# Kernel optimization log

Hardware: AMD Instinct MI355X
Metric: run time of the kernel (lower is better)

The kernel has to match this reference:

```python
import jax, jax.numpy as jnp
import numpy as np

INPUT, HIDDEN = 8, 16

def setup_inputs() -> dict:
    key = jax.random.key(0)
    ks = jax.random.split(key, 7)
    s_ih = 1.0 / np.sqrt(HIDDEN)
    x = jax.random.normal(ks[0], (8192, 512, INPUT), dtype=jnp.float32)
    W_ih = jax.random.uniform(ks[1], (HIDDEN, INPUT), jnp.float32, -s_ih, s_ih)
    W_hh = jax.random.uniform(ks[2], (HIDDEN, HIDDEN), jnp.float32, -s_ih, s_ih)
    b_ih = jax.random.uniform(ks[3], (HIDDEN,), jnp.float32, -s_ih, s_ih)
    b_hh = jax.random.uniform(ks[4], (HIDDEN,), jnp.float32, -s_ih, s_ih)
    s_fc = 1.0 / np.sqrt(HIDDEN)
    fc_w = jax.random.uniform(ks[5], (1, HIDDEN), jnp.float32, -s_fc, s_fc)
    fc_b = jax.random.uniform(ks[6], (1,), jnp.float32, -s_fc, s_fc)
    return {"x": x, "W_ih": W_ih, "W_hh": W_hh, "b_ih": b_ih, "b_hh": b_hh, "fc_w": fc_w, "fc_b": fc_b}

def reference(x, W_ih, W_hh, b_ih, b_hh, fc_w, fc_b):
    B, T, _ = x.shape
    # Precompute input projection for all timesteps: [B, T, H]
    xp = jnp.einsum('bti,hi->bth', x, W_ih) + b_ih + b_hh
    h0 = jnp.zeros((B, HIDDEN), dtype=x.dtype)

    def step(h, xt):
        h_new = jnp.tanh(xt + h @ W_hh.T)
        return h_new, None

    h_last, _ = jax.lax.scan(step, h0, jnp.swapaxes(xp, 0, 1))
    return h_last @ fc_w.T + fc_b  # [B, 1]
```

## Files before the change

### kernel.cpp

```cpp
#include <hip/hip_runtime.h>


#define RNN_B   8192
#define RNN_T   512
#define RNN_IN  8
#define RNN_H   16
#define TC      32
#define NB      16
#define XSTRIDE 264
#define HP      20

__global__ __launch_bounds__(256, 2) void rnn_fused_kernel(
    const float* __restrict__ x,
    const float* __restrict__ W_ih,
    const float* __restrict__ W_hh,
    const float* __restrict__ b_ih,
    const float* __restrict__ b_hh,
    const float* __restrict__ fc_w,
    const float* __restrict__ fc_b,
    float* __restrict__ out)
{
    __shared__ float xs[NB * XSTRIDE];
    __shared__ float hbuf[NB * HP];

    const int tid = (int)threadIdx.x;
    const int j   = tid & 15;
    const int g   = tid >> 4;
    const int b0  = (int)blockIdx.x * NB;
    const int b   = b0 + g;

    float whh[RNN_H];
#pragma unroll
    for (int k = 0; k < RNN_H; k += 4) {
        float4 w = *(const float4*)(W_hh + j * RNN_H + k);
        whh[k] = w.x; whh[k+1] = w.y; whh[k+2] = w.z; whh[k+3] = w.w;
    }
    float wih[RNN_IN];
#pragma unroll
    for (int i = 0; i < RNN_IN; i += 4) {
        float4 w = *(const float4*)(W_ih + j * RNN_IN + i);
        wih[i] = w.x; wih[i+1] = w.y; wih[i+2] = w.z; wih[i+3] = w.w;
    }
    const float bias = b_ih[j] + b_hh[j];

    hbuf[g * HP + j] = 0.0f;

    float hlast = 0.0f;

    for (int t0 = 0; t0 < RNN_T; t0 += TC) {
        __syncthreads();
#pragma unroll
        for (int p = 0; p < 4; ++p) {
            int idx = tid + p * 256;
            int row = idx >> 6;
            int off = idx & 63;
            float4 v = *(const float4*)(x + ((size_t)(b0 + row) * RNN_T + t0) * RNN_IN + off * 4);
            *(float4*)(xs + row * XSTRIDE + off * 4) = v;
        }
        __syncthreads();

#pragma unroll 4
        for (int tt = 0; tt < TC; ++tt) {
            const float* xp = xs + g * XSTRIDE + tt * RNN_IN;
            const float4 xa = *(const float4*)(xp);
            const float4 xb = *(const float4*)(xp + 4);
            const float4 h0 = *(const float4*)(hbuf + g * HP + 0);
            const float4 h1 = *(const float4*)(hbuf + g * HP + 4);
            const float4 h2 = *(const float4*)(hbuf + g * HP + 8);
            const float4 h3 = *(const float4*)(hbuf + g * HP + 12);

            float a0 = fmaf(wih[0], xa.x, bias);
            a0 = fmaf(wih[1], xa.y, a0);
            a0 = fmaf(wih[2], xa.z, a0);
            a0 = fmaf(wih[3], xa.w, a0);
            a0 = fmaf(whh[0], h0.x, a0);
            a0 = fmaf(whh[1], h0.y, a0);

            float a1 = wih[4] * xb.x;
            a1 = fmaf(wih[5], xb.y, a1);
            a1 = fmaf(wih[6], xb.z, a1);
            a1 = fmaf(wih[7], xb.w, a1);
            a1 = fmaf(whh[2], h0.z, a1);
            a1 = fmaf(whh[3], h0.w, a1);

            float a2 = whh[4] * h1.x;
            a2 = fmaf(whh[5],  h1.y, a2);
            a2 = fmaf(whh[6],  h1.z, a2);
            a2 = fmaf(whh[7],  h1.w, a2);
            a2 = fmaf(whh[8],  h2.x, a2);
            a2 = fmaf(whh[9],  h2.y, a2);

            float a3 = whh[10] * h2.z;
            a3 = fmaf(whh[11], h2.w, a3);
            a3 = fmaf(whh[12], h3.x, a3);
            a3 = fmaf(whh[13], h3.y, a3);
            a3 = fmaf(whh[14], h3.z, a3);
            a3 = fmaf(whh[15], h3.w, a3);

            const float s = (a0 + a1) + (a2 + a3);

            const float e  = __expf(s + s);
            const float r  = __builtin_amdgcn_rcpf(e + 1.0f);
            const float hn = fmaf(-2.0f, r, 1.0f);

            hbuf[g * HP + j] = hn;
            hlast = hn;
        }
    }

    float v = hlast * fc_w[j];
    v += __shfl_xor(v, 1);
    v += __shfl_xor(v, 2);
    v += __shfl_xor(v, 4);
    v += __shfl_xor(v, 8);
    if (j == 0) out[b] = v + fc_b[0];
}

extern "C" void kernel_launch(void* const* d_in, const int* in_sizes, int n_in,
                              void* d_out, int out_size, void* d_ws, size_t ws_size,
                              hipStream_t stream)
{
    const float* x    = (const float*)d_in[0];
    const float* W_ih = (const float*)d_in[1];
    const float* W_hh = (const float*)d_in[2];
    const float* b_ih = (const float*)d_in[3];
    const float* b_hh = (const float*)d_in[4];
    const float* fc_w = (const float*)d_in[5];
    const float* fc_b = (const float*)d_in[6];
    float* out = (float*)d_out;

    dim3 grid(RNN_B / NB);
    dim3 block(256);
    rnn_fused_kernel<<<grid, block, 0, stream>>>(x, W_ih, W_hh, b_ih, b_hh, fc_w, fc_b, out);
}
```

Before: 239.2 us.

## Rewrite RNN recurrence as per-wave fp16 MFMA with split-precision and async staging

Replaces the scalar FMA recurrence (one thread per hidden unit, shared-memory hidden state) with a single-wavefront-per-block kernel that computes each timestep as two 16x16x32 fp16 MFMAs. Hidden state and weights use hi/lo fp16 splitting to keep accuracy, and tanh is re-expressed as a sigmoid-style exp2/rcp form with its constants folded into the weights and bias. Input tiles are double-buffered through global_load_lds so loading overlaps compute, and the hidden state is exchanged with ds_bpermute instead of LDS stores. The cost is fp16 rounding error through 512 recurrent steps and much smaller blocks, which lowers per-block parallelism.

Result: slower. 266.6 us (+11.4%).

```diff
diff --git a/kernel.cpp b/kernel.cpp
--- a/kernel.cpp
+++ b/kernel.cpp
@@ -1,4 +1,5 @@
 #include <hip/hip_runtime.h>
+#include <stdint.h>
 
 
 #define RNN_B   8192
@@ -6,11 +7,41 @@
 #define RNN_IN  8
 #define RNN_H   16
 #define TC      32
-#define NB      16
-#define XSTRIDE 264
-#define HP      20
+#define NE      16
+#define XROW    260
+#define NTILE   (RNN_T / TC)
+#define BUFSZ   (NE * XROW)
 
-__global__ __launch_bounds__(256, 2) void rnn_fused_kernel(
+typedef __fp16 half8  __attribute__((ext_vector_type(8)));
+typedef __fp16 half2v __attribute__((ext_vector_type(2)));
+typedef float  f32x4  __attribute__((ext_vector_type(4)));
+
+union H8U { half8 v; __fp16 e[8]; uint32_t u[4]; };
+union H2U { half2v h; uint32_t u; };
+
+static __device__ __forceinline__ uint32_t pkh(float a, float b) {
+    H2U t; t.h = __builtin_amdgcn_cvt_pkrtz(a, b); return t.u;
+}
+static __device__ __forceinline__ uint32_t bp32(int addr, uint32_t v) {
+    return (uint32_t)__builtin_amdgcn_ds_bpermute(addr, (int)v);
+}
+
+static __device__ __forceinline__ void stage(const float* __restrict__ x,
+                                             float* lds_base, int b0, int t0,
+                                             int lane)
+{
+#pragma unroll
+    for (int e = 0; e < NE; ++e) {
+        const float* gp = x + ((size_t)(b0 + e) * RNN_T + t0) * RNN_IN + lane * 4;
+        float* lp = lds_base + e * XROW;
+        __builtin_amdgcn_global_load_lds(
+            (const __attribute__((address_space(1))) uint32_t*)gp,
+            (__attribute__((address_space(3))) uint32_t*)lp,
+            16, 0, 0);
+    }
+}
+
+__global__ __launch_bounds__(64) void rnn_mfma_kernel(
     const float* __restrict__ x,
     const float* __restrict__ W_ih,
     const float* __restrict__ W_hh,
@@ -20,100 +51,105 @@
     const float* __restrict__ fc_b,
     float* __restrict__ out)
 {
-    __shared__ float xs[NB * XSTRIDE];
-    __shared__ float hbuf[NB * HP];
+    __shared__ __align__(16) float xs[2 * BUFSZ];
 
-    const int tid = (int)threadIdx.x;
-    const int j   = tid & 15;
-    const int g   = tid >> 4;
-    const int b0  = (int)blockIdx.x * NB;
-    const int b   = b0 + g;
+    const int lane = (int)threadIdx.x;
+    const int col  = lane & 15;
+    const int q    = lane >> 4;
+    const int b0   = (int)blockIdx.x * NE;
+    const bool hi32  = (lane & 32) != 0;
+    const int addr32 = (lane ^ 32) << 2;
+    const float C2 = 2.8853900817779268f;
 
-    float whh[RNN_H];
+    H8U A1, A2;
 #pragma unroll
-    for (int k = 0; k < RNN_H; k += 4) {
-        float4 w = *(const float4*)(W_hh + j * RNN_H + k);
-        whh[k] = w.x; whh[k+1] = w.y; whh[k+2] = w.z; whh[k+3] = w.w;
+    for (int j = 0; j < 8; ++j) {
+        const int i = j >> 1, hb = j & 1;
+        const int u = 4 * ((i < 2) ? q : (q ^ 2)) + 2 * (i & 1) + hb;
+        const float v = -2.0f * C2 * W_hh[col * RNN_H + u];
+        const __fp16 vh = (__fp16)v;
+        A1.e[j] = vh;
+        if (q < 2) A2.e[j] = (__fp16)(v - (float)vh);
     }
-    float wih[RNN_IN];
+    if (q >= 2) {
 #pragma unroll
-    for (int i = 0; i < RNN_IN; i += 4) {
-        float4 w = *(const float4*)(W_ih + j * RNN_IN + i);
-        wih[i] = w.x; wih[i+1] = w.y; wih[i+2] = w.z; wih[i+3] = w.w;
+        for (int j = 0; j < 8; ++j) {
+            const float uu = C2 * W_ih[col * RNN_IN + j];
+            const __fp16 uh = (__fp16)uu;
+            A2.e[j] = (q == 2) ? uh : (__fp16)(uu - (float)uh);
+        }
     }
-    const float bias = b_ih[j] + b_hh[j];
 
-    hbuf[g * HP + j] = 0.0f;
+    f32x4 cb;
+#pragma unroll
+    for (int rr = 0; rr < 4; ++rr) {
+        const int u = 4 * q + rr;
+        float s = 0.0f;
+        for (int k = 0; k < RNN_H; ++k) {
+            const float v = -2.0f * C2 * W_hh[u * RNN_H + k];
+            const __fp16 vh = (__fp16)v;
+            const __fp16 vl = (__fp16)(v - (float)vh);
+            s += (float)vh + (float)vl;
+        }
+        cb[rr] = C2 * (b_ih[u] + b_hh[u]) - 0.5f * s;
+    }
 
-    float hlast = 0.0f;
+    stage(x, xs, b0, 0, lane);
+    __syncthreads();
 
-    for (int t0 = 0; t0 < RNN_T; t0 += TC) {
-        __syncthreads();
-#pragma unroll
-        for (int p = 0; p < 4; ++p) {
-            int idx = tid + p * 256;
-            int row = idx >> 6;
-            int off = idx & 63;
-            float4 v = *(const float4*)(x + ((size_t)(b0 + row) * RNN_T + t0) * RNN_IN + off * 4);
-            *(float4*)(xs + row * XSTRIDE + off * 4) = v;
-        }
-        __syncthreads();
+    uint32_t rh0 = pkh(0.5f, 0.5f), rh1 = pkh(0.5f, 0.5f);
+    uint32_t rl0 = 0u, rl1 = 0u;
+
+    for (int tile = 0; tile < NTILE; ++tile) {
+        const int cur = tile & 1;
+        if (tile + 1 < NTILE)
+            stage(x, xs + (cur ^ 1) * BUFSZ, b0, (tile + 1) * TC, lane);
+
+        const float* xg = xs + cur * BUFSZ + col * XROW;
 
 #pragma unroll 4
         for (int tt = 0; tt < TC; ++tt) {
-            const float* xp = xs + g * XSTRIDE + tt * RNN_IN;
-            const float4 xa = *(const float4*)(xp);
-            const float4 xb = *(const float4*)(xp + 4);
-            const float4 h0 = *(const float4*)(hbuf + g * HP + 0);
-            const float4 h1 = *(const float4*)(hbuf + g * HP + 4);
-            const float4 h2 = *(const float4*)(hbuf + g * HP + 8);
-            const float4 h3 = *(const float4*)(hbuf + g * HP + 12);
+            const float4 xa = *(const float4*)(xg + tt * 8);
+            const float4 xb = *(const float4*)(xg + tt * 8 + 4);
+            const uint32_t xh0 = pkh(xa.x, xa.y), xh1 = pkh(xa.z, xa.w);
+            const uint32_t xh2 = pkh(xb.x, xb.y), xh3 = pkh(xb.z, xb.w);
 
-            float a0 = fmaf(wih[0], xa.x, bias);
-            a0 = fmaf(wih[1], xa.y, a0);
-            a0 = fmaf(wih[2], xa.z, a0);
-            a0 = fmaf(wih[3], xa.w, a0);
-            a0 = fmaf(whh[0], h0.x, a0);
-            a0 = fmaf(whh[1], h0.y, a0);
+            const uint32_t G0h = bp32(addr32, rh0), G1h = bp32(addr32, rh1);
+            const uint32_t G0l = bp32(addr32, rl0), G1l = bp32(addr32, rl1);
 
-            float a1 = wih[4] * xb.x;
-            a1 = fmaf(wih[5], xb.y, a1);
-            a1 = fmaf(wih[6], xb.z, a1);
-            a1 = fmaf(wih[7], xb.w, a1);
-            a1 = fmaf(whh[2], h0.z, a1);
-            a1 = fmaf(whh[3], h0.w, a1);
+            H8U B1, B2;
+            B1.u[0] = hi32 ? rl0 : rh0;  B1.u[1] = hi32 ? rl1 : rh1;
+            B1.u[2] = hi32 ? G0l : G0h;  B1.u[3] = hi32 ? G1l : G1h;
+            B2.u[0] = hi32 ? xh0 : rh0;  B2.u[1] = hi32 ? xh1 : rh1;
+            B2.u[2] = hi32 ? xh2 : G0h;  B2.u[3] = hi32 ? xh3 : G1h;
 
-            float a2 = whh[4] * h1.x;
-            a2 = fmaf(whh[5],  h1.y, a2);
-            a2 = fmaf(whh[6],  h1.z, a2);
-            a2 = fmaf(whh[7],  h1.w, a2);
-            a2 = fmaf(whh[8],  h2.x, a2);
-            a2 = fmaf(whh[9],  h2.y, a2);
+            f32x4 acc = __builtin_amdgcn_mfma_f32_16x16x32_f16(A1.v, B1.v, cb, 0, 0, 0);
+            acc = __builtin_amdgcn_mfma_f32_16x16x32_f16(A2.v, B2.v, acc, 0, 0, 0);
 
-            float a3 = whh[10] * h2.z;
-            a3 = fmaf(whh[11], h2.w, a3);
-            a3 = fmaf(whh[12], h3.x, a3);
-            a3 = fmaf(whh[13], h3.y, a3);
-            a3 = fmaf(whh[14], h3.z, a3);
-            a3 = fmaf(whh[15], h3.w, a3);
+            const float r0 = __builtin_amdgcn_rcpf(__builtin_amdgcn_exp2f(acc[0]) + 1.0f);
+            const float r1 = __builtin_amdgcn_rcpf(__builtin_amdgcn_exp2f(acc[1]) + 1.0f);
+            const float r2 = __builtin_amdgcn_rcpf(__builtin_amdgcn_exp2f(acc[2]) + 1.0f);
+            const float r3 = __builtin_amdgcn_rcpf(__builtin_amdgcn_exp2f(acc[3]) + 1.0f);
 
-            const float s = (a0 + a1) + (a2 + a3);
-
-            const float e  = __expf(s + s);
-            const float r  = __builtin_amdgcn_rcpf(e + 1.0f);
-            const float hn = fmaf(-2.0f, r, 1.0f);
-
-            hbuf[g * HP + j] = hn;
-            hlast = hn;
+            rh0 = pkh(r0, r1); rh1 = pkh(r2, r3);
+            H2U u0, u1; u0.u = rh0; u1.u = rh1;
+            rl0 = pkh(r0 - (float)u0.h[0], r1 - (float)u0.h[1]);
+            rl1 = pkh(r2 - (float)u1.h[0], r3 - (float)u1.h[1]);
         }
+        __syncthreads();
     }
 
-    float v = hlast * fc_w[j];
-    v += __shfl_xor(v, 1);
-    v += __shfl_xor(v, 2);
-    v += __shfl_xor(v, 4);
-    v += __shfl_xor(v, 8);
-    if (j == 0) out[b] = v + fc_b[0];
+    H2U a0, a1, c0, c1;
+    a0.u = rh0; a1.u = rh1; c0.u = rl0; c1.u = rl1;
+    const float h0 = 1.0f - 2.0f * ((float)a0.h[0] + (float)c0.h[0]);
+    const float h1 = 1.0f - 2.0f * ((float)a0.h[1] + (float)c0.h[1]);
+    const float h2 = 1.0f - 2.0f * ((float)a1.h[0] + (float)c1.h[0]);
+    const float h3 = 1.0f - 2.0f * ((float)a1.h[1] + (float)c1.h[1]);
+    float p = fc_w[4 * q + 0] * h0 + fc_w[4 * q + 1] * h1
+            + fc_w[4 * q + 2] * h2 + fc_w[4 * q + 3] * h3;
+    p += __shfl_xor(p, 16);
+    p += __shfl_xor(p, 32);
+    if (lane < 16) out[b0 + col] = p + fc_b[0];
 }
 
 extern "C" void kernel_launch(void* const* d_in, const int* in_sizes, int n_in,
@@ -129,7 +165,7 @@
     const float* fc_b = (const float*)d_in[6];
     float* out = (float*)d_out;
 
-    dim3 grid(RNN_B / NB);
-    dim3 block(256);
-    rnn_fused_kernel<<<grid, block, 0, stream>>>(x, W_ih, W_hh, b_ih, b_hh, fc_w, fc_b, out);
+    dim3 grid(RNN_B / NE);
+    dim3 block(64);
+    rnn_mfma_kernel<<<grid, block, 0, stream>>>(x, W_ih, W_hh, b_ih, b_hh, fc_w, fc_b, out);
 }
```
